# Kernel tuning notes

Hardware: AMD Instinct MI355X
Metric: run time of the kernel (lower is better)

## Reference

```python
import jax, jax.numpy as jnp
import numpy as np

VOCAB, D, T, NC = 21128, 768, 4, 10
B, S = 64, 512


def setup_inputs() -> dict:
    key = jax.random.key(0)
    ks = jax.random.split(key, 12)
    inv = 1.0 / np.sqrt(D)
    return {
        "words": jax.random.randint(ks[0], (B, S), 0, VOCAB),
        "target": jax.random.randint(ks[1], (B, S), 0, T),
        "corpus": jax.random.randint(ks[2], (B,), 0, NC),
        "embed_table": jax.random.normal(ks[3], (VOCAB, D), jnp.float32) * 0.02,
        "shared_W": jax.random.uniform(ks[4], (D, T), jnp.float32, -inv, inv),
        "shared_b": jax.random.uniform(ks[5], (T,), jnp.float32, -inv, inv),
        "domain_A": jax.random.uniform(ks[6], (NC, D, T), jnp.float32, -inv, inv),
        "domain_b": jax.random.uniform(ks[7], (NC, T), jnp.float32, -inv, inv),
        "trans_m": jax.random.normal(ks[8], (T, T), jnp.float32) * 0.1,
        "start_scores": jax.random.normal(ks[9], (T,), jnp.float32) * 0.1,
        "end_scores": jax.random.normal(ks[10], (T,), jnp.float32) * 0.1,
    }


def reference(words, target, corpus, embed_table, shared_W, shared_b,
              domain_A, domain_b, trans_m, start_scores, end_scores):
    mask = words != 0                                    # (B,S) pad mask
    x = embed_table[words]                               # (B,S,D) embedding lookup
    # domain-gated projection: shared linear + per-corpus bmm
    out1 = jnp.einsum('bsd,dt->bst', x, shared_W) + shared_b
    A = domain_A[corpus]                                 # (B,D,T)
    bb = domain_b[corpus][:, None, :]                    # (B,1,T)
    out2 = jnp.einsum('bsd,bdt->bst', x, A) + bb
    logits = jax.nn.log_softmax(out1 + out2, axis=-1)    # (B,S,T)

    # --- CRF normalizer (forward algorithm, logsumexp scan over time) ---
    alpha0 = logits[:, 0] + start_scores[None, :]        # (B,T)

    def step(alpha, inp):
        logit_t, m_t = inp                               # (B,T), (B,)
        tmp = alpha[:, :, None] + logit_t[:, None, :] + trans_m[None, :, :]
        new = jax.nn.logsumexp(tmp, axis=1)              # (B,T)
        return jnp.where(m_t[:, None], new, alpha), None

    xs = (jnp.swapaxes(logits[:, 1:], 0, 1), jnp.swapaxes(mask[:, 1:], 0, 1))
    alpha, _ = jax.lax.scan(step, alpha0, xs)
    normalizer = jax.nn.logsumexp(alpha + end_scores[None, :], axis=1)  # (B,)

    # --- gold path score ---
    emit = jnp.take_along_axis(logits, target[..., None], axis=-1)[..., 0]  # (B,S)
    emit = jnp.where(mask, emit, 0.0)
    tr = trans_m[target[:, :-1], target[:, 1:]]          # (B,S-1)
    tr = jnp.where(mask[:, 1:], tr, 0.0)
    last_idx = jnp.maximum(jnp.sum(mask.astype(jnp.int32), axis=1) - 1, 0)
    bidx = jnp.arange(words.shape[0])
    gold = (emit.sum(1) + tr.sum(1)
            + start_scores[target[:, 0]]
            + end_scores[target[bidx, last_idx]])
    return normalizer - gold                             # (B,) NLL per sequence
```

## Files before the change

kernel.cpp:

```cpp
#include <hip/hip_runtime.h>

#define NB 64
#define NS 512
#define ND 768
#define NT 4
#define NEG (-1e30f)

__global__ __launch_bounds__(256, 4) void logits_kernel(
    const int* __restrict__ words, const int* __restrict__ corpus,
    const float* __restrict__ embed, const float* __restrict__ sW,
    const float* __restrict__ sb, const float* __restrict__ dA,
    const float* __restrict__ db, float* __restrict__ logits)
{
  const int lane = threadIdx.x & 63;
  const int wv   = threadIdx.x >> 6;
  const int b    = blockIdx.x >> 3;
  const int sblk = (blockIdx.x & 7) * 64;
  const int c    = corpus[b];

  float4 w[3][4];
  const float4* sW4 = (const float4*)sW;
  const float4* dA4 = (const float4*)(dA + (size_t)c * ND * NT);
#pragma unroll
  for (int ch = 0; ch < 3; ++ch) {
#pragma unroll
    for (int q = 0; q < 4; ++q) {
      const int d = ch * 256 + lane * 4 + q;
      const float4 a = sW4[d];
      const float4 e = dA4[d];
      w[ch][q] = make_float4(a.x + e.x, a.y + e.y, a.z + e.z, a.w + e.w);
    }
  }
  float4 bias;
  {
    const float4 a = *(const float4*)sb;
    const float4 e = *(const float4*)(db + c * NT);
    bias = make_float4(a.x + e.x, a.y + e.y, a.z + e.z, a.w + e.w);
  }

#pragma unroll 2
  for (int i = 0; i < 16; ++i) {
    const int s = sblk + i * 4 + wv;
    const int word = words[b * NS + s];
    const float4* x4 = (const float4*)(embed + (size_t)word * ND);
    float a0 = 0.f, a1 = 0.f, a2 = 0.f, a3 = 0.f;
#pragma unroll
    for (int ch = 0; ch < 3; ++ch) {
      const float4 xv = x4[ch * 64 + lane];
      a0 = fmaf(xv.x, w[ch][0].x, a0); a1 = fmaf(xv.x, w[ch][0].y, a1);
      a2 = fmaf(xv.x, w[ch][0].z, a2); a3 = fmaf(xv.x, w[ch][0].w, a3);
      a0 = fmaf(xv.y, w[ch][1].x, a0); a1 = fmaf(xv.y, w[ch][1].y, a1);
      a2 = fmaf(xv.y, w[ch][1].z, a2); a3 = fmaf(xv.y, w[ch][1].w, a3);
      a0 = fmaf(xv.z, w[ch][2].x, a0); a1 = fmaf(xv.z, w[ch][2].y, a1);
      a2 = fmaf(xv.z, w[ch][2].z, a2); a3 = fmaf(xv.z, w[ch][2].w, a3);
      a0 = fmaf(xv.w, w[ch][3].x, a0); a1 = fmaf(xv.w, w[ch][3].y, a1);
      a2 = fmaf(xv.w, w[ch][3].z, a2); a3 = fmaf(xv.w, w[ch][3].w, a3);
    }
#pragma unroll
    for (int off = 32; off; off >>= 1) {
      a0 += __shfl_xor(a0, off);
      a1 += __shfl_xor(a1, off);
      a2 += __shfl_xor(a2, off);
      a3 += __shfl_xor(a3, off);
    }
    if (lane == 0) {
      a0 += bias.x; a1 += bias.y; a2 += bias.z; a3 += bias.w;
      const float m = fmaxf(fmaxf(a0, a1), fmaxf(a2, a3));
      const float sum = __expf(a0 - m) + __expf(a1 - m) + __expf(a2 - m) + __expf(a3 - m);
      const float lse = m + __logf(sum);
      ((float4*)logits)[b * NS + s] = make_float4(a0 - lse, a1 - lse, a2 - lse, a3 - lse);
    }
  }
}

__global__ __launch_bounds__(256) void crf_kernel(
    const int* __restrict__ words, const int* __restrict__ target,
    const float* __restrict__ trans, const float* __restrict__ start_s,
    const float* __restrict__ end_s, const float* __restrict__ logits,
    float* __restrict__ out)
{
  const int tid = threadIdx.x;
  const int b = blockIdx.x;
  const int c = tid >> 2;
  const int a = tid & 3;

  __shared__ float bufA[64][16];
  __shared__ float bufB[32][16];
  __shared__ float wg[4];
  __shared__ int   wc[4];

  const float* lg = logits + (size_t)b * NS * NT;
  const int* wb = words + b * NS;
  const int* tb = target + b * NS;

  float gp = 0.f; int cp = 0;
#pragma unroll
  for (int q = 0; q < 2; ++q) {
    const int s = tid * 2 + q;
    if (wb[s] != 0) {
      const int t = tb[s];
      gp += lg[s * 4 + t];
      if (s > 0) gp += trans[tb[s - 1] * 4 + t];
      ++cp;
    }
  }
#pragma unroll
  for (int off = 32; off; off >>= 1) {
    gp += __shfl_xor(gp, off);
    cp += __shfl_xor(cp, off);
  }
  if ((tid & 63) == 0) { wg[tid >> 6] = gp; wc[tid >> 6] = cp; }

  float T[4][4];
#pragma unroll
  for (int i = 0; i < 4; ++i)
#pragma unroll
    for (int j = 0; j < 4; ++j) T[i][j] = trans[i * 4 + j];

  const int s_beg = 1 + c * 8;
  float4 lv[8]; int wm[8];
#pragma unroll
  for (int q = 0; q < 8; ++q) {
    const int s = s_beg + q;
    const bool in = s < NS;
    wm[q] = in ? wb[s] : 0;
    lv[q] = in ? *(const float4*)(lg + s * 4) : make_float4(0.f, 0.f, 0.f, 0.f);
  }

  float v0 = (a == 0) ? 0.f : NEG;
  float v1 = (a == 1) ? 0.f : NEG;
  float v2 = (a == 2) ? 0.f : NEG;
  float v3 = (a == 3) ? 0.f : NEG;
#pragma unroll
  for (int q = 0; q < 8; ++q) {
    if (wm[q] != 0) {
      const float4 l = lv[q];
      float t0, t1, t2, t3, m, sm;
      float n0, n1, n2, n3;
      t0 = v0 + T[0][0]; t1 = v1 + T[1][0]; t2 = v2 + T[2][0]; t3 = v3 + T[3][0];
      m = fmaxf(fmaxf(t0, t1), fmaxf(t2, t3));
      sm = __expf(t0 - m) + __expf(t1 - m) + __expf(t2 - m) + __expf(t3 - m);
      n0 = m + __logf(sm) + l.x;
      t0 = v0 + T[0][1]; t1 = v1 + T[1][1]; t2 = v2 + T[2][1]; t3 = v3 + T[3][1];
      m = fmaxf(fmaxf(t0, t1), fmaxf(t2, t3));
      sm = __expf(t0 - m) + __expf(t1 - m) + __expf(t2 - m) + __expf(t3 - m);
      n1 = m + __logf(sm) + l.y;
      t0 = v0 + T[0][2]; t1 = v1 + T[1][2]; t2 = v2 + T[2][2]; t3 = v3 + T[3][2];
      m = fmaxf(fmaxf(t0, t1), fmaxf(t2, t3));
      sm = __expf(t0 - m) + __expf(t1 - m) + __expf(t2 - m) + __expf(t3 - m);
      n2 = m + __logf(sm) + l.z;
      t0 = v0 + T[0][3]; t1 = v1 + T[1][3]; t2 = v2 + T[2][3]; t3 = v3 + T[3][3];
      m = fmaxf(fmaxf(t0, t1), fmaxf(t2, t3));
      sm = __expf(t0 - m) + __expf(t1 - m) + __expf(t2 - m) + __expf(t3 - m);
      n3 = m + __logf(sm) + l.w;
      v0 = n0; v1 = n1; v2 = n2; v3 = n3;
    }
  }
  bufA[c][a * 4 + 0] = v0;
  bufA[c][a * 4 + 1] = v1;
  bufA[c][a * 4 + 2] = v2;
  bufA[c][a * 4 + 3] = v3;

  float* src = &bufA[0][0];
  float* dst = &bufB[0][0];
  for (int n = 64; n > 1; n >>= 1) {
    const int entries = (n >> 1) * 16;
    __syncthreads();
    for (int e = tid; e < entries; e += 256) {
      const int p = e >> 4;
      const int aa = (e >> 2) & 3;
      const int jj = e & 3;
      const float* C1 = src + (2 * p) * 16;
      const float* C2 = src + (2 * p + 1) * 16;
      const float t0 = C1[aa * 4 + 0] + C2[0 * 4 + jj];
      const float t1 = C1[aa * 4 + 1] + C2[1 * 4 + jj];
      const float t2 = C1[aa * 4 + 2] + C2[2 * 4 + jj];
      const float t3 = C1[aa * 4 + 3] + C2[3 * 4 + jj];
      const float m = fmaxf(fmaxf(t0, t1), fmaxf(t2, t3));
      dst[p * 16 + aa * 4 + jj] =
          m + __logf(__expf(t0 - m) + __expf(t1 - m) + __expf(t2 - m) + __expf(t3 - m));
    }
    float* tmp = src; src = dst; dst = tmp;
  }
  __syncthreads();

  if (tid == 0) {
    const float* C = &bufA[0][0];
    const float4 l0 = *(const float4*)lg;
    const float a0 = l0.x + start_s[0];
    const float a1 = l0.y + start_s[1];
    const float a2 = l0.z + start_s[2];
    const float a3 = l0.w + start_s[3];
    float af[4];
#pragma unroll
    for (int j = 0; j < 4; ++j) {
      const float t0 = a0 + C[0 * 4 + j];
      const float t1 = a1 + C[1 * 4 + j];
      const float t2 = a2 + C[2 * 4 + j];
      const float t3 = a3 + C[3 * 4 + j];
      const float m = fmaxf(fmaxf(t0, t1), fmaxf(t2, t3));
      af[j] = m + __logf(__expf(t0 - m) + __expf(t1 - m) + __expf(t2 - m) + __expf(t3 - m));
    }
    const float z0 = af[0] + end_s[0], z1 = af[1] + end_s[1];
    const float z2 = af[2] + end_s[2], z3 = af[3] + end_s[3];
    const float mz = fmaxf(fmaxf(z0, z1), fmaxf(z2, z3));
    const float norm = mz + __logf(__expf(z0 - mz) + __expf(z1 - mz) +
                                   __expf(z2 - mz) + __expf(z3 - mz));

    float gold = wg[0] + wg[1] + wg[2] + wg[3];
    const int cnt = wc[0] + wc[1] + wc[2] + wc[3];
    const int last = (cnt - 1) > 0 ? (cnt - 1) : 0;
    gold += start_s[tb[0]] + end_s[tb[last]];
    out[b] = norm - gold;
  }
}

extern "C" void kernel_launch(void* const* d_in, const int* in_sizes, int n_in,
                              void* d_out, int out_size, void* d_ws, size_t ws_size,
                              hipStream_t stream) {
  const int*   words   = (const int*)d_in[0];
  const int*   target  = (const int*)d_in[1];
  const int*   corpus  = (const int*)d_in[2];
  const float* embed   = (const float*)d_in[3];
  const float* sW      = (const float*)d_in[4];
  const float* sb      = (const float*)d_in[5];
  const float* dA      = (const float*)d_in[6];
  const float* db      = (const float*)d_in[7];
  const float* trans   = (const float*)d_in[8];
  const float* start_s = (const float*)d_in[9];
  const float* end_s   = (const float*)d_in[10];
  float* out = (float*)d_out;
  float* logits = (float*)d_ws;

  logits_kernel<<<NB * 8, 256, 0, stream>>>(words, corpus, embed, sW, sb, dA, db, logits);
  crf_kernel<<<NB, 256, 0, stream>>>(words, target, trans, start_s, end_s, logits, out);
}
```

Before: 36.58 us.

## Map one thread per token and precompute per-corpus effective weights

Adds a small kernel that precombines shared and domain weights and biases for every corpus. The logits kernel now assigns one token per thread: each thread walks its whole embedding row and reads the weights as wave-uniform scalar loads. This removes the cross-lane shuffle reduction and the per-block weight setup. In exchange, each lane reads a different row, so the loads are uncoalesced, and there is an extra kernel launch.

```diff
diff --git a/kernel.cpp b/kernel.cpp
--- a/kernel.cpp
+++ b/kernel.cpp
@@ -4,73 +4,59 @@
 #define NS 512
 #define ND 768
 #define NT 4
+#define NC 10
 #define NEG (-1e30f)
 
-__global__ __launch_bounds__(256, 4) void logits_kernel(
+__global__ void weff_kernel(const float* __restrict__ sW,
+                            const float* __restrict__ dA,
+                            const float* __restrict__ sb,
+                            const float* __restrict__ db,
+                            float* __restrict__ weff,
+                            float* __restrict__ beff)
+{
+  const int i = blockIdx.x * 256 + threadIdx.x;
+  if (i < NC * ND * NT) weff[i] = sW[i % (ND * NT)] + dA[i];
+  if (i < NC * NT)      beff[i] = sb[i & 3] + db[i];
+}
+
+__global__ __launch_bounds__(64) void logits_kernel(
     const int* __restrict__ words, const int* __restrict__ corpus,
-    const float* __restrict__ embed, const float* __restrict__ sW,
-    const float* __restrict__ sb, const float* __restrict__ dA,
-    const float* __restrict__ db, float* __restrict__ logits)
+    const float* __restrict__ embed, const float* __restrict__ weff,
+    const float* __restrict__ beff, float* __restrict__ logits)
 {
-  const int lane = threadIdx.x & 63;
-  const int wv   = threadIdx.x >> 6;
-  const int b    = blockIdx.x >> 3;
-  const int sblk = (blockIdx.x & 7) * 64;
-  const int c    = corpus[b];
-
-  float4 w[3][4];
-  const float4* sW4 = (const float4*)sW;
-  const float4* dA4 = (const float4*)(dA + (size_t)c * ND * NT);
-#pragma unroll
-  for (int ch = 0; ch < 3; ++ch) {
-#pragma unroll
-    for (int q = 0; q < 4; ++q) {
-      const int d = ch * 256 + lane * 4 + q;
-      const float4 a = sW4[d];
-      const float4 e = dA4[d];
-      w[ch][q] = make_float4(a.x + e.x, a.y + e.y, a.z + e.z, a.w + e.w);
-    }
-  }
-  float4 bias;
-  {
-    const float4 a = *(const float4*)sb;
-    const float4 e = *(const float4*)(db + c * NT);
-    bias = make_float4(a.x + e.x, a.y + e.y, a.z + e.z, a.w + e.w);
-  }
-
+  const int lane = threadIdx.x;
+  const int g = blockIdx.x * 64 + lane;
+  const int b = g >> 9;
+  const int c = __builtin_amdgcn_readfirstlane(corpus[b]);
+  const float* __restrict__ w = weff + c * (ND * NT);
+
+  const int word = words[g];
+  const float* __restrict__ row = embed + (size_t)word * ND;
+
+  float a0 = 0.f, a1 = 0.f, a2 = 0.f, a3 = 0.f;
 #pragma unroll 2
-  for (int i = 0; i < 16; ++i) {
-    const int s = sblk + i * 4 + wv;
-    const int word = words[b * NS + s];
-    const float4* x4 = (const float4*)(embed + (size_t)word * ND);
-    float a0 = 0.f, a1 = 0.f, a2 = 0.f, a3 = 0.f;
-#pragma unroll
-    for (int ch = 0; ch < 3; ++ch) {
-      const float4 xv = x4[ch * 64 + lane];
-      a0 = fmaf(xv.x, w[ch][0].x, a0); a1 = fmaf(xv.x, w[ch][0].y, a1);
-      a2 = fmaf(xv.x, w[ch][0].z, a2); a3 = fmaf(xv.x, w[ch][0].w, a3);
-      a0 = fmaf(xv.y, w[ch][1].x, a0); a1 = fmaf(xv.y, w[ch][1].y, a1);
-      a2 = fmaf(xv.y, w[ch][1].z, a2); a3 = fmaf(xv.y, w[ch][1].w, a3);
-      a0 = fmaf(xv.z, w[ch][2].x, a0); a1 = fmaf(xv.z, w[ch][2].y, a1);
-      a2 = fmaf(xv.z, w[ch][2].z, a2); a3 = fmaf(xv.z, w[ch][2].w, a3);
-      a0 = fmaf(xv.w, w[ch][3].x, a0); a1 = fmaf(xv.w, w[ch][3].y, a1);
-      a2 = fmaf(xv.w, w[ch][3].z, a2); a3 = fmaf(xv.w, w[ch][3].w, a3);
-    }
-#pragma unroll
-    for (int off = 32; off; off >>= 1) {
-      a0 += __shfl_xor(a0, off);
-      a1 += __shfl_xor(a1, off);
-      a2 += __shfl_xor(a2, off);
-      a3 += __shfl_xor(a3, off);
-    }
-    if (lane == 0) {
-      a0 += bias.x; a1 += bias.y; a2 += bias.z; a3 += bias.w;
-      const float m = fmaxf(fmaxf(a0, a1), fmaxf(a2, a3));
-      const float sum = __expf(a0 - m) + __expf(a1 - m) + __expf(a2 - m) + __expf(a3 - m);
-      const float lse = m + __logf(sum);
-      ((float4*)logits)[b * NS + s] = make_float4(a0 - lse, a1 - lse, a2 - lse, a3 - lse);
-    }
-  }
+  for (int d0 = 0; d0 < ND; d0 += 16) {
+    float xs[16];
+    *(float4*)(xs + 0)  = *(const float4*)(row + d0 + 0);
+    *(float4*)(xs + 4)  = *(const float4*)(row + d0 + 4);
+    *(float4*)(xs + 8)  = *(const float4*)(row + d0 + 8);
+    *(float4*)(xs + 12) = *(const float4*)(row + d0 + 12);
+    const float* __restrict__ wc = w + d0 * NT;
+#pragma unroll
+    for (int q = 0; q < 16; ++q) {
+      a0 = fmaf(xs[q], wc[q * 4 + 0], a0);
+      a1 = fmaf(xs[q], wc[q * 4 + 1], a1);
+      a2 = fmaf(xs[q], wc[q * 4 + 2], a2);
+      a3 = fmaf(xs[q], wc[q * 4 + 3], a3);
+    }
+  }
+
+  const float* __restrict__ be = beff + c * NT;
+  a0 += be[0]; a1 += be[1]; a2 += be[2]; a3 += be[3];
+  const float m = fmaxf(fmaxf(a0, a1), fmaxf(a2, a3));
+  const float sum = __expf(a0 - m) + __expf(a1 - m) + __expf(a2 - m) + __expf(a3 - m);
+  const float lse = m + __logf(sum);
+  ((float4*)logits)[g] = make_float4(a0 - lse, a1 - lse, a2 - lse, a3 - lse);
 }
 
 __global__ __launch_bounds__(256) void crf_kernel(
@@ -230,8 +216,12 @@
   const float* start_s = (const float*)d_in[9];
   const float* end_s   = (const float*)d_in[10];
   float* out = (float*)d_out;
+
   float* logits = (float*)d_ws;
-
-  logits_kernel<<<NB * 8, 256, 0, stream>>>(words, corpus, embed, sW, sb, dA, db, logits);
+  float* weff   = logits + (size_t)NB * NS * NT;
+  float* beff   = weff + NC * ND * NT;
+
+  weff_kernel<<<(NC * ND * NT + 255) / 256, 256, 0, stream>>>(sW, dA, sb, db, weff, beff);
+  logits_kernel<<<(NB * NS) / 64, 64, 0, stream>>>(words, corpus, embed, weff, beff, logits);
   crf_kernel<<<NB, 256, 0, stream>>>(words, target, trans, start_s, end_s, logits, out);
 }
```

Result: slower. 45.91 us (+25.5%).

## Restructure logits kernel: 16 tokens per block, weights in LDS, 16-lane groups

Applied to the files above, without the earlier changes.

The logits kernel now launches 2048 blocks of 16 tokens each, up from 512 blocks of 64 tokens. Each block stages the combined shared and domain weights into LDS. Each 16-lane group handles one token, reading its 768-dim row across 12 float4 loads with a shorter 4-step shuffle reduction. This aims for more parallelism and more embedding loads in flight, so the gather latency is better hidden, at the cost of rebuilding the weight matrix in every block and adding LDS reads per FMA.

```diff
diff --git a/kernel.cpp b/kernel.cpp
--- a/kernel.cpp
+++ b/kernel.cpp
@@ -4,72 +4,80 @@
 #define NS 512
 #define ND 768
 #define NT 4
+#define NC 10
 #define NEG (-1e30f)
 
-__global__ __launch_bounds__(256, 4) void logits_kernel(
+__global__ __launch_bounds__(256) void logits_kernel(
     const int* __restrict__ words, const int* __restrict__ corpus,
     const float* __restrict__ embed, const float* __restrict__ sW,
     const float* __restrict__ sb, const float* __restrict__ dA,
     const float* __restrict__ db, float* __restrict__ logits)
 {
-  const int lane = threadIdx.x & 63;
-  const int wv   = threadIdx.x >> 6;
-  const int b    = blockIdx.x >> 3;
-  const int sblk = (blockIdx.x & 7) * 64;
-  const int c    = corpus[b];
-
-  float4 w[3][4];
+  __shared__ float4 Wl[ND];
+  __shared__ float4 bl;
+
+  const int tid = threadIdx.x;
+  const int blk = blockIdx.x;
+  const int b = blk >> 5;
+  const int c = __builtin_amdgcn_readfirstlane(corpus[b]);
+
   const float4* sW4 = (const float4*)sW;
-  const float4* dA4 = (const float4*)(dA + (size_t)c * ND * NT);
-#pragma unroll
-  for (int ch = 0; ch < 3; ++ch) {
-#pragma unroll
-    for (int q = 0; q < 4; ++q) {
-      const int d = ch * 256 + lane * 4 + q;
-      const float4 a = sW4[d];
-      const float4 e = dA4[d];
-      w[ch][q] = make_float4(a.x + e.x, a.y + e.y, a.z + e.z, a.w + e.w);
-    }
-  }
-  float4 bias;
-  {
+  const float4* dA4 = ((const float4*)dA) + (size_t)c * ND;
+#pragma unroll
+  for (int k = 0; k < 3; ++k) {
+    const int d = tid + k * 256;
+    const float4 a = sW4[d];
+    const float4 e = dA4[d];
+    Wl[d] = make_float4(a.x + e.x, a.y + e.y, a.z + e.z, a.w + e.w);
+  }
+  if (tid == 0) {
     const float4 a = *(const float4*)sb;
-    const float4 e = *(const float4*)(db + c * NT);
-    bias = make_float4(a.x + e.x, a.y + e.y, a.z + e.z, a.w + e.w);
-  }
-
-#pragma unroll 2
-  for (int i = 0; i < 16; ++i) {
-    const int s = sblk + i * 4 + wv;
-    const int word = words[b * NS + s];
-    const float4* x4 = (const float4*)(embed + (size_t)word * ND);
-    float a0 = 0.f, a1 = 0.f, a2 = 0.f, a3 = 0.f;
-#pragma unroll
-    for (int ch = 0; ch < 3; ++ch) {
-      const float4 xv = x4[ch * 64 + lane];
-      a0 = fmaf(xv.x, w[ch][0].x, a0); a1 = fmaf(xv.x, w[ch][0].y, a1);
-      a2 = fmaf(xv.x, w[ch][0].z, a2); a3 = fmaf(xv.x, w[ch][0].w, a3);
-      a0 = fmaf(xv.y, w[ch][1].x, a0); a1 = fmaf(xv.y, w[ch][1].y, a1);
-      a2 = fmaf(xv.y, w[ch][1].z, a2); a3 = fmaf(xv.y, w[ch][1].w, a3);
-      a0 = fmaf(xv.z, w[ch][2].x, a0); a1 = fmaf(xv.z, w[ch][2].y, a1);
-      a2 = fmaf(xv.z, w[ch][2].z, a2); a3 = fmaf(xv.z, w[ch][2].w, a3);
-      a0 = fmaf(xv.w, w[ch][3].x, a0); a1 = fmaf(xv.w, w[ch][3].y, a1);
-      a2 = fmaf(xv.w, w[ch][3].z, a2); a3 = fmaf(xv.w, w[ch][3].w, a3);
-    }
-#pragma unroll
-    for (int off = 32; off; off >>= 1) {
-      a0 += __shfl_xor(a0, off);
-      a1 += __shfl_xor(a1, off);
-      a2 += __shfl_xor(a2, off);
-      a3 += __shfl_xor(a3, off);
-    }
-    if (lane == 0) {
-      a0 += bias.x; a1 += bias.y; a2 += bias.z; a3 += bias.w;
-      const float m = fmaxf(fmaxf(a0, a1), fmaxf(a2, a3));
-      const float sum = __expf(a0 - m) + __expf(a1 - m) + __expf(a2 - m) + __expf(a3 - m);
-      const float lse = m + __logf(sum);
-      ((float4*)logits)[b * NS + s] = make_float4(a0 - lse, a1 - lse, a2 - lse, a3 - lse);
-    }
+    const float4 e = ((const float4*)db)[c];
+    bl = make_float4(a.x + e.x, a.y + e.y, a.z + e.z, a.w + e.w);
+  }
+  __syncthreads();
+
+  const int lane = tid & 63;
+  const int grp  = lane >> 4;
+  const int q    = lane & 15;
+  const int g    = blk * 16 + (tid >> 6) * 4 + grp;
+
+  const int word = words[g];
+  const float4* __restrict__ row4 = (const float4*)(embed + (size_t)word * ND);
+
+  float a0 = 0.f, a1 = 0.f, a2 = 0.f, a3 = 0.f;
+#pragma unroll
+  for (int i = 0; i < 12; ++i) {
+    const float4 xv = row4[i * 16 + q];
+    const float4 w0 = Wl[i * 64 + q * 4 + 0];
+    const float4 w1 = Wl[i * 64 + q * 4 + 1];
+    const float4 w2 = Wl[i * 64 + q * 4 + 2];
+    const float4 w3 = Wl[i * 64 + q * 4 + 3];
+    a0 = fmaf(xv.x, w0.x, a0); a1 = fmaf(xv.x, w0.y, a1);
+    a2 = fmaf(xv.x, w0.z, a2); a3 = fmaf(xv.x, w0.w, a3);
+    a0 = fmaf(xv.y, w1.x, a0); a1 = fmaf(xv.y, w1.y, a1);
+    a2 = fmaf(xv.y, w1.z, a2); a3 = fmaf(xv.y, w1.w, a3);
+    a0 = fmaf(xv.z, w2.x, a0); a1 = fmaf(xv.z, w2.y, a1);
+    a2 = fmaf(xv.z, w2.z, a2); a3 = fmaf(xv.z, w2.w, a3);
+    a0 = fmaf(xv.w, w3.x, a0); a1 = fmaf(xv.w, w3.y, a1);
+    a2 = fmaf(xv.w, w3.z, a2); a3 = fmaf(xv.w, w3.w, a3);
+  }
+
+#pragma unroll
+  for (int off = 8; off; off >>= 1) {
+    a0 += __shfl_xor(a0, off);
+    a1 += __shfl_xor(a1, off);
+    a2 += __shfl_xor(a2, off);
+    a3 += __shfl_xor(a3, off);
+  }
+
+  if (q == 0) {
+    a0 += bl.x; a1 += bl.y; a2 += bl.z; a3 += bl.w;
+    const float m = fmaxf(fmaxf(a0, a1), fmaxf(a2, a3));
+    const float sum = __expf(a0 - m) + __expf(a1 - m) +
+                      __expf(a2 - m) + __expf(a3 - m);
+    const float lse = m + __logf(sum);
+    ((float4*)logits)[g] = make_float4(a0 - lse, a1 - lse, a2 - lse, a3 - lse);
   }
 }
 
@@ -232,6 +240,6 @@
   float* out = (float*)d_out;
   float* logits = (float*)d_ws;
 
-  logits_kernel<<<NB * 8, 256, 0, stream>>>(words, corpus, embed, sW, sb, dA, db, logits);
+  logits_kernel<<<(NB * NS) / 16, 256, 0, stream>>>(words, corpus, embed, sW, sb, dA, db, logits);
   crf_kernel<<<NB, 256, 0, stream>>>(words, target, trans, start_s, end_s, logits, out);
 }
```

New measurement: 30.51 us. 16.6% less time.
